# Kernel tuning notes

Measured on AMD Instinct MI355X. Metric: run time of the kernel, lower is better.

The kernel has to match this reference:

```python
import jax, jax.numpy as jnp
import numpy as np

B, S, D, H, P = 4, 4096, 1024, 8, 32
K = D // H  # head_dim = 128


def setup_inputs() -> dict:
    key = jax.random.key(0)
    ks = jax.random.split(key, 12)
    f = lambda k, shape, s: jax.random.normal(k, shape, dtype=jnp.float32) * s
    return {
        "x": f(ks[0], (B, S, D), 1.0),
        "W_proj": f(ks[1], (H, K, D), 0.03),
        "resonance_freqs": f(ks[2], (H, K), 0.01),
        "pol_W": f(ks[3], (H, P, K), 0.08),
        "pol_b": jnp.zeros((H, P), jnp.float32),
        "imp_W1": f(ks[4], (16, 1), 0.5),               # Linear(1, 16)
        "imp_b1": jnp.zeros((16,), jnp.float32),
        "imp_W2": f(ks[5], (1, 16), 0.25),              # Linear(16, 1)
        "imp_b2": jnp.zeros((1,), jnp.float32),
        "out_W": f(ks[6], (D, D), 0.03),                # Linear(dim, dim)
        "out_b": jnp.zeros((D,), jnp.float32),
        "ln_g": jnp.ones((D,), jnp.float32),
        "ln_b": jnp.zeros((D,), jnp.float32),
        "causal": 1,
    }


def reference(x, W_proj, resonance_freqs, pol_W, pol_b, imp_W1, imp_b1,
              imp_W2, imp_b2, out_W, out_b, ln_g, ln_b, causal):
    Bx, Sx, Dx = x.shape
    nH = W_proj.shape[0]
    # per-head projection + resonance frequency modulation -> (B, H, S, K)
    heads = jnp.einsum('bsd,hkd->bhsk', x, W_proj)
    heads = heads * jnp.cos(resonance_freqs * jnp.pi)[None, :, None, :]

    # --- GuaXiangDuiChong: learned cross-head impedance ---
    summary = heads.mean(axis=2)                                   # (B, H, K)
    pol = jnp.tanh(jnp.einsum('bhk,hpk->bhp', summary, pol_W) + pol_b[None])
    pol = pol / jnp.maximum(jnp.linalg.norm(pol, axis=-1, keepdims=True), 1e-12)
    dots = jnp.einsum('bhp,bgp->bhg', pol, pol)                    # (B, H, H)
    z = dots[..., None]                                            # (B, H, H, 1)
    hid = jax.nn.gelu(z * imp_W1[:, 0] + imp_b1, approximate=False)  # (B, H, H, 16)
    imp = jax.nn.softplus(jnp.einsum('bijc,oc->bijo', hid, imp_W2) + imp_b2)[..., 0]
    eye = jnp.eye(nH, dtype=x.dtype)
    impedance = imp * (1.0 - eye)                                  # (B, H, H)

    # --- cross-head transfer ---
    # h_i += sum_{j != i} heads_j / (1 + imp[i,j]) * 0.1, causally mean-masked.
    coef = (0.1 / (1.0 + impedance)) * (1.0 - eye)                 # zero diagonal (i == j skipped)
    transfer = jnp.einsum('bij,bjsk->bisk', coef, heads)           # (B, H, S, K)
    if causal and Sx > 1:
        # masked_fill(t>s)+mean over t of a key-independent tensor == scale by (s+1)/S
        scale = (jnp.arange(Sx, dtype=x.dtype) + 1.0) / Sx
        transfer = transfer * scale[None, None, :, None]
    out_heads = heads + transfer

    merged = out_heads.transpose(0, 2, 1, 3).reshape(Bx, Sx, Dx)   # cat heads on last dim
    y = merged @ out_W.T + out_b + x                               # dropout is identity in eval
    mu = y.mean(-1, keepdims=True)
    var = ((y - mu) ** 2).mean(-1, keepdims=True)
    normed = (y - mu) / jnp.sqrt(var + 1e-5) * ln_g + ln_b
    return normed, impedance
```

## Files before the change

kernel.cpp:

```cpp
#include <hip/hip_runtime.h>

typedef __bf16 bf16x8 __attribute__((ext_vector_type(8)));
typedef float f32x4 __attribute__((ext_vector_type(4)));

#define PI_F 3.14159265358979323846f

__device__ __forceinline__ unsigned short f2bf(float f) {
    unsigned u = __float_as_uint(f);
    u += 0x7FFFu + ((u >> 16) & 1u);
    return (unsigned short)(u >> 16);
}
__device__ __forceinline__ float bf2f(unsigned short h) {
    return __uint_as_float(((unsigned)h) << 16);
}

__device__ __forceinline__ void async16(const void* g, void* l) {
    __builtin_amdgcn_global_load_lds(
        (const __attribute__((address_space(1))) unsigned int*)g,
        (__attribute__((address_space(3))) unsigned int*)l, 16, 0, 0);
}

__global__ __launch_bounds__(256) void prep_w1(const float* __restrict__ W,
                                               const float* __restrict__ fr,
                                               unsigned short* __restrict__ W1b) {
    int idx = blockIdx.x * 256 + threadIdx.x;
    int n = idx >> 10, d = idx & 1023;
    int k = n >> 3, h = n & 7;
    float c = cosf(fr[h * 128 + k] * PI_F);
    W1b[idx] = f2bf(W[((h * 128 + k) << 10) + d] * c);
}

__global__ __launch_bounds__(256) void prep_wo(const float* __restrict__ Wo,
                                               unsigned short* __restrict__ Wob) {
    int idx = blockIdx.x * 256 + threadIdx.x;
    int n = idx >> 10, dp = idx & 1023;
    int k = dp >> 3, h = dp & 7;
    Wob[idx] = f2bf(Wo[(n << 10) + h * 128 + k]);
}

__global__ __launch_bounds__(256) void xbar_cast(const float* __restrict__ x,
                                                 unsigned short* __restrict__ xb,
                                                 float* __restrict__ xbar) {
    int bid = blockIdx.x;
    int b = bid >> 7;
    int s0 = (bid & 127) * 32;
    int t = threadIdx.x;
    float a0 = 0.f, a1 = 0.f, a2 = 0.f, a3 = 0.f;
    for (int i = 0; i < 32; ++i) {
        long row = (long)b * 4096 + s0 + i;
        float4 v = ((const float4*)x)[row * 256 + t];
        a0 += v.x; a1 += v.y; a2 += v.z; a3 += v.w;
        ushort4 u;
        u.x = f2bf(v.x); u.y = f2bf(v.y); u.z = f2bf(v.z); u.w = f2bf(v.w);
        ((ushort4*)xb)[row * 256 + t] = u;
    }
    float* xr = xbar + b * 1024 + t * 4;
    atomicAdd(xr + 0, a0); atomicAdd(xr + 1, a1);
    atomicAdd(xr + 2, a2); atomicAdd(xr + 3, a3);
}

__global__ __launch_bounds__(256) void summary_k(const float* __restrict__ xbar,
                                                 const float* __restrict__ W,
                                                 const float* __restrict__ fr,
                                                 float* __restrict__ summary) {
    int wave = (blockIdx.x * 256 + threadIdx.x) >> 6;
    int lane = threadIdx.x & 63;
    int b = wave >> 10, hk = wave & 1023;
    int h = hk >> 7, k = hk & 127;
    const float* wrow = &W[(h * 128 + k) << 10];
    const float* xrow = &xbar[b << 10];
    float s = 0.f;
    for (int d = lane; d < 1024; d += 64) s += xrow[d] * wrow[d];
    for (int off = 32; off; off >>= 1) s += __shfl_down(s, off);
    if (lane == 0) {
        float c = cosf(fr[h * 128 + k] * PI_F);
        summary[wave] = s * c * (1.0f / 4096.0f);
    }
}

__global__ __launch_bounds__(256) void imp_k(const float* __restrict__ summary,
                                             const float* __restrict__ pol_W,
                                             const float* __restrict__ pol_b,
                                             const float* __restrict__ imp_W1,
                                             const float* __restrict__ imp_b1,
                                             const float* __restrict__ imp_W2,
                                             const float* __restrict__ imp_b2,
                                             float* __restrict__ coef_out,
                                             float* __restrict__ imp_out) {
    __shared__ float pol[4][8][32];
    __shared__ float rn[32];
    int t = threadIdx.x;
    for (int o = t; o < 1024; o += 256) {
        int b = o >> 8, h = (o >> 5) & 7, p = o & 31;
        const float* srow = &summary[(b * 8 + h) * 128];
        const float* wrow = &pol_W[(h * 32 + p) * 128];
        float acc = pol_b[h * 32 + p];
        for (int k = 0; k < 128; ++k) acc += srow[k] * wrow[k];
        pol[b][h][p] = tanhf(acc);
    }
    __syncthreads();
    if (t < 32) {
        int b = t >> 3, h = t & 7;
        float ss = 0.f;
        for (int p = 0; p < 32; ++p) { float v = pol[b][h][p]; ss += v * v; }
        rn[t] = 1.0f / fmaxf(sqrtf(ss), 1e-12f);
    }
    __syncthreads();
    {
        int b = t >> 6, i = (t >> 3) & 7, j = t & 7;
        float d = 0.f;
        for (int p = 0; p < 32; ++p) d += pol[b][i][p] * pol[b][j][p];
        d *= rn[b * 8 + i] * rn[b * 8 + j];
        float s = imp_b2[0];
        for (int c = 0; c < 16; ++c) {
            float z = d * imp_W1[c] + imp_b1[c];
            float gl = 0.5f * z * (1.0f + erff(z * 0.70710678118654752f));
            s += gl * imp_W2[c];
        }
        float sp = fmaxf(s, 0.0f) + log1pf(expf(-fabsf(s)));
        float impv = (i == j) ? 0.0f : sp;
        imp_out[t] = impv;
        coef_out[t] = (i == j) ? 0.0f : 0.1f / (1.0f + impv);
    }
}

__global__ __launch_bounds__(256, 3) void gemm_bt(const unsigned short* __restrict__ A,
                                                  const unsigned short* __restrict__ B,
                                                  unsigned short* __restrict__ C) {
    __shared__ unsigned short As[128 * 32];
    __shared__ unsigned short Bs[128 * 32];
    const int t = threadIdx.x;
    const int wave = t >> 6;
    const int lane = t & 63;
    const int wr = wave >> 1, wc = wave & 1;
    const long rowBase = (long)blockIdx.y * 128;
    const long colBase = (long)blockIdx.x * 128;

    const int lr = lane >> 2;
    const int lb = (lane & 3) * 16;
    const char* gA = (const char*)A + (rowBase + wave * 32 + lr) * 2048 + lb;
    const char* gB = (const char*)B + (colBase + wave * 32 + lr) * 2048 + lb;
    char* lA = (char*)As + wave * 2048;
    char* lB = (char*)Bs + wave * 2048;
    const int q = lane >> 4;
    const int c16 = lane & 15;

    f32x4 acc[4][4] = {};
    for (int kt = 0; kt < 1024; kt += 32) {
        const char* a0 = gA + kt * 2;
        const char* b0 = gB + kt * 2;
        async16(a0, lA);
        async16(a0 + 16 * 2048, lA + 1024);
        async16(b0, lB);
        async16(b0 + 16 * 2048, lB + 1024);
        __syncthreads();
        bf16x8 af[4], bfr[4];
#pragma unroll
        for (int mi = 0; mi < 4; ++mi)
            af[mi] = *(const bf16x8*)((const char*)As + ((wr * 64 + mi * 16 + c16) * 32 + q * 8) * 2);
#pragma unroll
        for (int ni = 0; ni < 4; ++ni)
            bfr[ni] = *(const bf16x8*)((const char*)Bs + ((wc * 64 + ni * 16 + c16) * 32 + q * 8) * 2);
#pragma unroll
        for (int mi = 0; mi < 4; ++mi)
#pragma unroll
            for (int ni = 0; ni < 4; ++ni)
                acc[mi][ni] = __builtin_amdgcn_mfma_f32_16x16x32_bf16(af[mi], bfr[ni], acc[mi][ni], 0, 0, 0);
        __syncthreads();
    }
#pragma unroll
    for (int mi = 0; mi < 4; ++mi) {
#pragma unroll
        for (int ni = 0; ni < 4; ++ni) {
            long col = colBase + wc * 64 + ni * 16 + c16;
            long row0 = rowBase + wr * 64 + mi * 16 + q * 4;
#pragma unroll
            for (int r = 0; r < 4; ++r)
                C[(row0 + r) * 1024 + col] = f2bf(acc[mi][ni][r]);
        }
    }
}

__global__ __launch_bounds__(256) void mix_k(const unsigned short* __restrict__ heads,
                                             const float* __restrict__ coef,
                                             const int* __restrict__ causal,
                                             unsigned short* __restrict__ merged) {
    __shared__ float cf[256];
    int t = threadIdx.x;
    cf[t] = coef[t];
    __syncthreads();
    long g = (long)blockIdx.x * 256 + t;
    long bs = g >> 7;
    int m = (int)(g & 127);
    int b = (int)(bs >> 12);
    int s = (int)(bs & 4095);
    float scale = causal[0] ? (float)(s + 1) * (1.0f / 4096.0f) : 1.0f;
    const ushort4* hp = (const ushort4*)(heads + bs * 1024 + m * 8);
    ushort4 u0 = hp[0], u1 = hp[1];
    float v[8] = {bf2f(u0.x), bf2f(u0.y), bf2f(u0.z), bf2f(u0.w),
                  bf2f(u1.x), bf2f(u1.y), bf2f(u1.z), bf2f(u1.w)};
    const float* cb = cf + b * 64;
    float o[8];
#pragma unroll
    for (int i = 0; i < 8; ++i) {
        float ts = 0.f;
#pragma unroll
        for (int j = 0; j < 8; ++j) ts += cb[i * 8 + j] * v[j];
        o[i] = v[i] + scale * ts;
    }
    ushort4 o0, o1;
    o0.x = f2bf(o[0]); o0.y = f2bf(o[1]); o0.z = f2bf(o[2]); o0.w = f2bf(o[3]);
    o1.x = f2bf(o[4]); o1.y = f2bf(o[5]); o1.z = f2bf(o[6]); o1.w = f2bf(o[7]);
    ushort4* op = (ushort4*)(merged + bs * 1024 + m * 8);
    op[0] = o0; op[1] = o1;
}

__global__ __launch_bounds__(256) void ln_k(const unsigned short* __restrict__ ypre,
                                            const float* __restrict__ x,
                                            const float* __restrict__ outb,
                                            const float* __restrict__ gam,
                                            const float* __restrict__ bet,
                                            float* __restrict__ out) {
    int row = blockIdx.x;
    int t = threadIdx.x;
    long base = (long)row * 1024 + t * 4;
    ushort4 yp = *(const ushort4*)(ypre + base);
    float4 xv = *(const float4*)(x + base);
    float4 bv = *(const float4*)(outb + t * 4);
    float y0 = bf2f(yp.x) + xv.x + bv.x;
    float y1 = bf2f(yp.y) + xv.y + bv.y;
    float y2 = bf2f(yp.z) + xv.z + bv.z;
    float y3 = bf2f(yp.w) + xv.w + bv.w;
    float s = y0 + y1 + y2 + y3;
    float ss = y0 * y0 + y1 * y1 + y2 * y2 + y3 * y3;
    for (int off = 32; off; off >>= 1) {
        s += __shfl_down(s, off);
        ss += __shfl_down(ss, off);
    }
    __shared__ float red[8];
    int wv = t >> 6, ln = t & 63;
    if (ln == 0) { red[wv] = s; red[4 + wv] = ss; }
    __syncthreads();
    if (t == 0) {
        float S1 = red[0] + red[1] + red[2] + red[3];
        float S2 = red[4] + red[5] + red[6] + red[7];
        float mu = S1 * (1.0f / 1024.0f);
        float var = S2 * (1.0f / 1024.0f) - mu * mu;
        red[0] = mu;
        red[1] = 1.0f / sqrtf(var + 1e-5f);
    }
    __syncthreads();
    float mu = red[0], rs = red[1];
    float4 gv = *(const float4*)(gam + t * 4);
    float4 bb = *(const float4*)(bet + t * 4);
    float4 o;
    o.x = (y0 - mu) * rs * gv.x + bb.x;
    o.y = (y1 - mu) * rs * gv.y + bb.y;
    o.z = (y2 - mu) * rs * gv.z + bb.z;
    o.w = (y3 - mu) * rs * gv.w + bb.w;
    *(float4*)(out + base) = o;
}

extern "C" void kernel_launch(void* const* d_in, const int* in_sizes, int n_in,
                              void* d_out, int out_size, void* d_ws, size_t ws_size,
                              hipStream_t stream) {
    const float* x       = (const float*)d_in[0];
    const float* W_proj  = (const float*)d_in[1];
    const float* freqs   = (const float*)d_in[2];
    const float* pol_W   = (const float*)d_in[3];
    const float* pol_b   = (const float*)d_in[4];
    const float* imp_W1  = (const float*)d_in[5];
    const float* imp_b1  = (const float*)d_in[6];
    const float* imp_W2  = (const float*)d_in[7];
    const float* imp_b2  = (const float*)d_in[8];
    const float* out_W   = (const float*)d_in[9];
    const float* out_b   = (const float*)d_in[10];
    const float* ln_g    = (const float*)d_in[11];
    const float* ln_b    = (const float*)d_in[12];
    const int*   causal  = (const int*)d_in[13];
    float* out = (float*)d_out;

    char* ws = (char*)d_ws;
    unsigned short* xb      = (unsigned short*)(ws + 0);
    unsigned short* heads   = (unsigned short*)(ws + 33554432);
    unsigned short* w1b     = (unsigned short*)(ws + 67108864);
    unsigned short* wob     = (unsigned short*)(ws + 69206016);
    float* xbar             = (float*)(ws + 71303168);
    float* summary          = (float*)(ws + 71319552);
    float* coef             = (float*)(ws + 71335936);
    unsigned short* merged  = xb;
    unsigned short* ypre    = heads;

    hipMemsetAsync(xbar, 0, 4096 * sizeof(float), stream);
    prep_w1<<<4096, 256, 0, stream>>>(W_proj, freqs, w1b);
    prep_wo<<<4096, 256, 0, stream>>>(out_W, wob);
    xbar_cast<<<512, 256, 0, stream>>>(x, xb, xbar);
    summary_k<<<1024, 256, 0, stream>>>(xbar, W_proj, freqs, summary);
    imp_k<<<1, 256, 0, stream>>>(summary, pol_W, pol_b, imp_W1, imp_b1,
                                 imp_W2, imp_b2, coef, out + 16777216);
    gemm_bt<<<dim3(8, 128), 256, 0, stream>>>(xb, w1b, heads);
    mix_k<<<8192, 256, 0, stream>>>(heads, coef, causal, merged);
    gemm_bt<<<dim3(8, 128), 256, 0, stream>>>(merged, wob, ypre);
    ln_k<<<16384, 256, 0, stream>>>(ypre, x, out_b, ln_g, ln_b, out);
}
```

Measured before the change: 319.9 us.

## Fuse head mixing into first GEMM epilogue, deepen K tile with swizzled LDS

```diff
diff --git a/kernel.cpp b/kernel.cpp
--- a/kernel.cpp
+++ b/kernel.cpp
@@ -2,6 +2,7 @@
 
 typedef __bf16 bf16x8 __attribute__((ext_vector_type(8)));
 typedef float f32x4 __attribute__((ext_vector_type(4)));
+typedef unsigned short us8 __attribute__((ext_vector_type(8)));
 
 #define PI_F 3.14159265358979323846f
 
@@ -20,33 +21,34 @@
         (__attribute__((address_space(3))) unsigned int*)l, 16, 0, 0);
 }
 
-__global__ __launch_bounds__(256) void prep_w1(const float* __restrict__ W,
-                                               const float* __restrict__ fr,
-                                               unsigned short* __restrict__ W1b) {
+__global__ __launch_bounds__(256) void prep_k(const float* __restrict__ W,
+                                              const float* __restrict__ fr,
+                                              const float* __restrict__ Wo,
+                                              unsigned short* __restrict__ W1b,
+                                              unsigned short* __restrict__ Wob) {
     int idx = blockIdx.x * 256 + threadIdx.x;
-    int n = idx >> 10, d = idx & 1023;
-    int k = n >> 3, h = n & 7;
-    float c = cosf(fr[h * 128 + k] * PI_F);
-    W1b[idx] = f2bf(W[((h * 128 + k) << 10) + d] * c);
-}
-
-__global__ __launch_bounds__(256) void prep_wo(const float* __restrict__ Wo,
-                                               unsigned short* __restrict__ Wob) {
-    int idx = blockIdx.x * 256 + threadIdx.x;
-    int n = idx >> 10, dp = idx & 1023;
-    int k = dp >> 3, h = dp & 7;
-    Wob[idx] = f2bf(Wo[(n << 10) + h * 128 + k]);
+    if (idx < (1 << 20)) {
+        int n = idx >> 10, d = idx & 1023;
+        int k = n >> 3, h = n & 7;
+        float c = cosf(fr[h * 128 + k] * PI_F);
+        W1b[idx] = f2bf(W[((h * 128 + k) << 10) + d] * c);
+    } else {
+        int i2 = idx - (1 << 20);
+        int n = i2 >> 10, dp = i2 & 1023;
+        int k = dp >> 3, h = dp & 7;
+        Wob[i2] = f2bf(Wo[(n << 10) + h * 128 + k]);
+    }
 }
 
 __global__ __launch_bounds__(256) void xbar_cast(const float* __restrict__ x,
                                                  unsigned short* __restrict__ xb,
                                                  float* __restrict__ xbar) {
     int bid = blockIdx.x;
-    int b = bid >> 7;
-    int s0 = (bid & 127) * 32;
+    int b = bid >> 9;
+    int s0 = (bid & 511) * 8;
     int t = threadIdx.x;
     float a0 = 0.f, a1 = 0.f, a2 = 0.f, a3 = 0.f;
-    for (int i = 0; i < 32; ++i) {
+    for (int i = 0; i < 8; ++i) {
         long row = (long)b * 4096 + s0 + i;
         float4 v = ((const float4*)x)[row * 256 + t];
         a0 += v.x; a1 += v.y; a2 += v.z; a3 += v.w;
@@ -124,50 +126,131 @@
     }
 }
 
+__device__ __forceinline__ void swizzle_blk(int n, long& rowBase, long& colBase) {
+    int xcd = n & 7, s = n >> 3;
+    rowBase = (long)(xcd * 16 + (s & 15)) * 128;
+    colBase = (long)(s >> 4) * 128;
+}
+
+#define GEMM_CORE(A_, B_, As_, Bs_)                                            \
+    const int wave = t >> 6;                                                   \
+    const int lane = t & 63;                                                   \
+    const int wr = wave >> 1, wc = wave & 1;                                   \
+    const int lr8 = lane >> 3;                             \
+    const int gr = lane & 7;                                      \
+    const int sw = ((gr ^ lr8) << 4);    \
+    const char* gA = (const char*)A_ + (rowBase + wave * 32 + lr8) * 2048 + sw;\
+    const char* gB = (const char*)B_ + (colBase + wave * 32 + lr8) * 2048 + sw;\
+    char* lA = (char*)As_ + wave * 4096;                                       \
+    char* lB = (char*)Bs_ + wave * 4096;                                       \
+    const int q = lane >> 4;                                                   \
+    const int c16 = lane & 15;                                                 \
+    const int xorm = c16 & 7;                                                  \
+    const int oA0 = ((q ^ xorm) << 4);                 \
+    const int oA1 = (((4 + q) ^ xorm) << 4);           \
+    const int aRow = (wr * 64 + c16) * 128;                                    \
+    const int bRow = (wc * 64 + c16) * 128;                                    \
+    f32x4 acc[4][4] = {};                                                      \
+    for (int kt = 0; kt < 2048; kt += 128) {                                   \
+        const char* a0 = gA + kt;                                              \
+        const char* b0 = gB + kt;                                              \
+        async16(a0, lA);                                                       \
+        async16(a0 + 8 * 2048, lA + 1024);                                     \
+        async16(a0 + 16 * 2048, lA + 2048);                                    \
+        async16(a0 + 24 * 2048, lA + 3072);                                    \
+        async16(b0, lB);                                                       \
+        async16(b0 + 8 * 2048, lB + 1024);                                     \
+        async16(b0 + 16 * 2048, lB + 2048);                                    \
+        async16(b0 + 24 * 2048, lB + 3072);                                    \
+        __syncthreads();                                                       \
+        bf16x8 af[2][4], bfr[2][4];                                            \
+        _Pragma("unroll")                                                      \
+        for (int mi = 0; mi < 4; ++mi) {                                       \
+            af[0][mi] = *(const bf16x8*)((const char*)As_ + aRow + mi * 2048 + oA0); \
+            af[1][mi] = *(const bf16x8*)((const char*)As_ + aRow + mi * 2048 + oA1); \
+        }                                                                      \
+        _Pragma("unroll")                                                      \
+        for (int ni = 0; ni < 4; ++ni) {                                       \
+            bfr[0][ni] = *(const bf16x8*)((const char*)Bs_ + bRow + ni * 2048 + oA0); \
+            bfr[1][ni] = *(const bf16x8*)((const char*)Bs_ + bRow + ni * 2048 + oA1); \
+        }                                                                      \
+        _Pragma("unroll")                                                      \
+        for (int h = 0; h < 2; ++h)                                            \
+            _Pragma("unroll")                                                  \
+            for (int mi = 0; mi < 4; ++mi)                                     \
+                _Pragma("unroll")                                              \
+                for (int ni = 0; ni < 4; ++ni)                                 \
+                    acc[mi][ni] = __builtin_amdgcn_mfma_f32_16x16x32_bf16(     \
+                        af[h][mi], bfr[h][ni], acc[mi][ni], 0, 0, 0);          \
+        __syncthreads();                                                       \
+    }
+
+__global__ __launch_bounds__(256, 3) void gemm1_mix(const unsigned short* __restrict__ A,
+                                                    const unsigned short* __restrict__ B,
+                                                    const float* __restrict__ coef,
+                                                    const int* __restrict__ causal,
+                                                    unsigned short* __restrict__ C) {
+    __shared__ float mixs[64 * 132];
+    __shared__ float cfs[64];
+    unsigned short* As = (unsigned short*)mixs;
+    unsigned short* Bs = As + 8192;
+    const int t = threadIdx.x;
+    long rowBase, colBase;
+    swizzle_blk(blockIdx.x, rowBase, colBase);
+    const int b = (int)(rowBase >> 12);
+    if (t < 64) cfs[t] = coef[b * 64 + t];
+    const int causalv = causal[0];
+
+    GEMM_CORE(A, B, As, Bs)
+
+#pragma unroll
+    for (int pass = 0; pass < 2; ++pass) {
+        if (wr == pass) {
+#pragma unroll
+            for (int mi = 0; mi < 4; ++mi)
+#pragma unroll
+                for (int ni = 0; ni < 4; ++ni)
+#pragma unroll
+                    for (int r = 0; r < 4; ++r)
+                        mixs[(mi * 16 + q * 4 + r) * 132 + wc * 64 + ni * 16 + c16] = acc[mi][ni][r];
+        }
+        __syncthreads();
+        long rb2 = rowBase + pass * 64;
+#pragma unroll
+        for (int it = 0; it < 4; ++it) {
+            int item = t + it * 256;
+            int r = item >> 4, kg = item & 15;
+            const float* src = mixs + r * 132 + kg * 8;
+            float v[8];
+#pragma unroll
+            for (int j = 0; j < 8; ++j) v[j] = src[j];
+            long row = rb2 + r;
+            float scale = causalv ? (float)((row & 4095) + 1) * (1.0f / 4096.0f) : 1.0f;
+            us8 o;
+#pragma unroll
+            for (int i = 0; i < 8; ++i) {
+                float ts = 0.f;
+#pragma unroll
+                for (int j = 0; j < 8; ++j) ts += cfs[i * 8 + j] * v[j];
+                o[i] = f2bf(v[i] + scale * ts);
+            }
+            *(us8*)(C + row * 1024 + colBase + kg * 8) = o;
+        }
+        __syncthreads();
+    }
+}
+
 __global__ __launch_bounds__(256, 3) void gemm_bt(const unsigned short* __restrict__ A,
                                                   const unsigned short* __restrict__ B,
                                                   unsigned short* __restrict__ C) {
-    __shared__ unsigned short As[128 * 32];
-    __shared__ unsigned short Bs[128 * 32];
+    __shared__ unsigned short As[128 * 64];
+    __shared__ unsigned short Bs[128 * 64];
     const int t = threadIdx.x;
-    const int wave = t >> 6;
-    const int lane = t & 63;
-    const int wr = wave >> 1, wc = wave & 1;
-    const long rowBase = (long)blockIdx.y * 128;
-    const long colBase = (long)blockIdx.x * 128;
-
-    const int lr = lane >> 2;
-    const int lb = (lane & 3) * 16;
-    const char* gA = (const char*)A + (rowBase + wave * 32 + lr) * 2048 + lb;
-    const char* gB = (const char*)B + (colBase + wave * 32 + lr) * 2048 + lb;
-    char* lA = (char*)As + wave * 2048;
-    char* lB = (char*)Bs + wave * 2048;
-    const int q = lane >> 4;
-    const int c16 = lane & 15;
-
-    f32x4 acc[4][4] = {};
-    for (int kt = 0; kt < 1024; kt += 32) {
-        const char* a0 = gA + kt * 2;
-        const char* b0 = gB + kt * 2;
-        async16(a0, lA);
-        async16(a0 + 16 * 2048, lA + 1024);
-        async16(b0, lB);
-        async16(b0 + 16 * 2048, lB + 1024);
-        __syncthreads();
-        bf16x8 af[4], bfr[4];
-#pragma unroll
-        for (int mi = 0; mi < 4; ++mi)
-            af[mi] = *(const bf16x8*)((const char*)As + ((wr * 64 + mi * 16 + c16) * 32 + q * 8) * 2);
-#pragma unroll
-        for (int ni = 0; ni < 4; ++ni)
-            bfr[ni] = *(const bf16x8*)((const char*)Bs + ((wc * 64 + ni * 16 + c16) * 32 + q * 8) * 2);
-#pragma unroll
-        for (int mi = 0; mi < 4; ++mi)
-#pragma unroll
-            for (int ni = 0; ni < 4; ++ni)
-                acc[mi][ni] = __builtin_amdgcn_mfma_f32_16x16x32_bf16(af[mi], bfr[ni], acc[mi][ni], 0, 0, 0);
-        __syncthreads();
-    }
+    long rowBase, colBase;
+    swizzle_blk(blockIdx.x, rowBase, colBase);
+
+    GEMM_CORE(A, B, As, Bs)
+
 #pragma unroll
     for (int mi = 0; mi < 4; ++mi) {
 #pragma unroll
@@ -179,40 +262,6 @@
                 C[(row0 + r) * 1024 + col] = f2bf(acc[mi][ni][r]);
         }
     }
-}
-
-__global__ __launch_bounds__(256) void mix_k(const unsigned short* __restrict__ heads,
-                                             const float* __restrict__ coef,
-                                             const int* __restrict__ causal,
-                                             unsigned short* __restrict__ merged) {
-    __shared__ float cf[256];
-    int t = threadIdx.x;
-    cf[t] = coef[t];
-    __syncthreads();
-    long g = (long)blockIdx.x * 256 + t;
-    long bs = g >> 7;
-    int m = (int)(g & 127);
-    int b = (int)(bs >> 12);
-    int s = (int)(bs & 4095);
-    float scale = causal[0] ? (float)(s + 1) * (1.0f / 4096.0f) : 1.0f;
-    const ushort4* hp = (const ushort4*)(heads + bs * 1024 + m * 8);
-    ushort4 u0 = hp[0], u1 = hp[1];
-    float v[8] = {bf2f(u0.x), bf2f(u0.y), bf2f(u0.z), bf2f(u0.w),
-                  bf2f(u1.x), bf2f(u1.y), bf2f(u1.z), bf2f(u1.w)};
-    const float* cb = cf + b * 64;
-    float o[8];
-#pragma unroll
-    for (int i = 0; i < 8; ++i) {
-        float ts = 0.f;
-#pragma unroll
-        for (int j = 0; j < 8; ++j) ts += cb[i * 8 + j] * v[j];
-        o[i] = v[i] + scale * ts;
-    }
-    ushort4 o0, o1;
-    o0.x = f2bf(o[0]); o0.y = f2bf(o[1]); o0.z = f2bf(o[2]); o0.w = f2bf(o[3]);
-    o1.x = f2bf(o[4]); o1.y = f2bf(o[5]); o1.z = f2bf(o[6]); o1.w = f2bf(o[7]);
-    ushort4* op = (ushort4*)(merged + bs * 1024 + m * 8);
-    op[0] = o0; op[1] = o1;
 }
 
 __global__ __launch_bounds__(256) void ln_k(const unsigned short* __restrict__ ypre,
@@ -282,24 +331,21 @@
 
     char* ws = (char*)d_ws;
     unsigned short* xb      = (unsigned short*)(ws + 0);
-    unsigned short* heads   = (unsigned short*)(ws + 33554432);
+    unsigned short* merged  = (unsigned short*)(ws + 33554432);
     unsigned short* w1b     = (unsigned short*)(ws + 67108864);
     unsigned short* wob     = (unsigned short*)(ws + 69206016);
     float* xbar             = (float*)(ws + 71303168);
     float* summary          = (float*)(ws + 71319552);
     float* coef             = (float*)(ws + 71335936);
-    unsigned short* merged  = xb;
-    unsigned short* ypre    = heads;
+    unsigned short* ypre    = xb;
 
     hipMemsetAsync(xbar, 0, 4096 * sizeof(float), stream);
-    prep_w1<<<4096, 256, 0, stream>>>(W_proj, freqs, w1b);
-    prep_wo<<<4096, 256, 0, stream>>>(out_W, wob);
-    xbar_cast<<<512, 256, 0, stream>>>(x, xb, xbar);
+    prep_k<<<8192, 256, 0, stream>>>(W_proj, freqs, out_W, w1b, wob);
+    xbar_cast<<<2048, 256, 0, stream>>>(x, xb, xbar);
     summary_k<<<1024, 256, 0, stream>>>(xbar, W_proj, freqs, summary);
     imp_k<<<1, 256, 0, stream>>>(summary, pol_W, pol_b, imp_W1, imp_b1,
                                  imp_W2, imp_b2, coef, out + 16777216);
-    gemm_bt<<<dim3(8, 128), 256, 0, stream>>>(xb, w1b, heads);
-    mix_k<<<8192, 256, 0, stream>>>(heads, coef, causal, merged);
-    gemm_bt<<<dim3(8, 128), 256, 0, stream>>>(merged, wob, ypre);
+    gemm1_mix<<<1024, 256, 0, stream>>>(xb, w1b, coef, causal, merged);
+    gemm_bt<<<1024, 256, 0, stream>>>(merged, wob, ypre);
     ln_k<<<16384, 256, 0, stream>>>(ypre, x, out_b, ln_g, ln_b, out);
 }
```

After: 403.2 us. 26.0% more time.

## Merge weight-prep kernels, replace atomic mean with two-stage reduction, swizzle GEMM tiles

Applied to the files above, without the earlier changes.

```diff
diff --git a/kernel.cpp b/kernel.cpp
--- a/kernel.cpp
+++ b/kernel.cpp
@@ -2,6 +2,7 @@
 
 typedef __bf16 bf16x8 __attribute__((ext_vector_type(8)));
 typedef float f32x4 __attribute__((ext_vector_type(4)));
+typedef unsigned short us8 __attribute__((ext_vector_type(8)));
 
 #define PI_F 3.14159265358979323846f
 
@@ -20,33 +21,34 @@
         (__attribute__((address_space(3))) unsigned int*)l, 16, 0, 0);
 }
 
-__global__ __launch_bounds__(256) void prep_w1(const float* __restrict__ W,
-                                               const float* __restrict__ fr,
-                                               unsigned short* __restrict__ W1b) {
+__global__ __launch_bounds__(256) void prep_k(const float* __restrict__ W,
+                                              const float* __restrict__ fr,
+                                              const float* __restrict__ Wo,
+                                              unsigned short* __restrict__ W1b,
+                                              unsigned short* __restrict__ Wob) {
     int idx = blockIdx.x * 256 + threadIdx.x;
-    int n = idx >> 10, d = idx & 1023;
-    int k = n >> 3, h = n & 7;
-    float c = cosf(fr[h * 128 + k] * PI_F);
-    W1b[idx] = f2bf(W[((h * 128 + k) << 10) + d] * c);
-}
-
-__global__ __launch_bounds__(256) void prep_wo(const float* __restrict__ Wo,
-                                               unsigned short* __restrict__ Wob) {
-    int idx = blockIdx.x * 256 + threadIdx.x;
-    int n = idx >> 10, dp = idx & 1023;
-    int k = dp >> 3, h = dp & 7;
-    Wob[idx] = f2bf(Wo[(n << 10) + h * 128 + k]);
+    if (idx < (1 << 20)) {
+        int n = idx >> 10, d = idx & 1023;
+        int k = n >> 3, h = n & 7;
+        float c = cosf(fr[h * 128 + k] * PI_F);
+        W1b[idx] = f2bf(W[((h * 128 + k) << 10) + d] * c);
+    } else {
+        int i2 = idx - (1 << 20);
+        int n = i2 >> 10, dp = i2 & 1023;
+        int k = dp >> 3, h = dp & 7;
+        Wob[i2] = f2bf(Wo[(n << 10) + h * 128 + k]);
+    }
 }
 
 __global__ __launch_bounds__(256) void xbar_cast(const float* __restrict__ x,
                                                  unsigned short* __restrict__ xb,
-                                                 float* __restrict__ xbar) {
+                                                 float* __restrict__ part) {
     int bid = blockIdx.x;
-    int b = bid >> 7;
-    int s0 = (bid & 127) * 32;
+    int b = bid >> 8;
+    int s0 = (bid & 255) * 16;
     int t = threadIdx.x;
     float a0 = 0.f, a1 = 0.f, a2 = 0.f, a3 = 0.f;
-    for (int i = 0; i < 32; ++i) {
+    for (int i = 0; i < 16; ++i) {
         long row = (long)b * 4096 + s0 + i;
         float4 v = ((const float4*)x)[row * 256 + t];
         a0 += v.x; a1 += v.y; a2 += v.z; a3 += v.w;
@@ -54,9 +56,26 @@
         u.x = f2bf(v.x); u.y = f2bf(v.y); u.z = f2bf(v.z); u.w = f2bf(v.w);
         ((ushort4*)xb)[row * 256 + t] = u;
     }
-    float* xr = xbar + b * 1024 + t * 4;
-    atomicAdd(xr + 0, a0); atomicAdd(xr + 1, a1);
-    atomicAdd(xr + 2, a2); atomicAdd(xr + 3, a3);
+    float4 p; p.x = a0; p.y = a1; p.z = a2; p.w = a3;
+    ((float4*)part)[bid * 256 + t] = p;
+}
+
+__global__ __launch_bounds__(256) void xbar_r(const float* __restrict__ part,
+                                              float* __restrict__ xbar) {
+    __shared__ float sl[256];
+    int blk = blockIdx.x;
+    int b = blk >> 3, dgrp = blk & 7;
+    int t = threadIdx.x;
+    int col = dgrp * 128 + (t & 127);
+    int ih = t >> 7;
+    float s = 0.f;
+    for (int i = 0; i < 128; ++i) {
+        int cb = b * 256 + ih * 128 + i;
+        s += part[cb * 1024 + col];
+    }
+    sl[t] = s;
+    __syncthreads();
+    if (t < 128) xbar[b * 1024 + col] = sl[t] + sl[t + 128];
 }
 
 __global__ __launch_bounds__(256) void summary_k(const float* __restrict__ xbar,
@@ -124,6 +143,12 @@
     }
 }
 
+__device__ __forceinline__ void swizzle_blk(int n, long& rowBase, long& colBase) {
+    int xcd = n & 7, s = n >> 3;
+    rowBase = (long)(xcd * 16 + (s & 15)) * 128;
+    colBase = (long)(s >> 4) * 128;
+}
+
 __global__ __launch_bounds__(256, 3) void gemm_bt(const unsigned short* __restrict__ A,
                                                   const unsigned short* __restrict__ B,
                                                   unsigned short* __restrict__ C) {
@@ -133,8 +158,8 @@
     const int wave = t >> 6;
     const int lane = t & 63;
     const int wr = wave >> 1, wc = wave & 1;
-    const long rowBase = (long)blockIdx.y * 128;
-    const long colBase = (long)blockIdx.x * 128;
+    long rowBase, colBase;
+    swizzle_blk(blockIdx.x, rowBase, colBase);
 
     const int lr = lane >> 2;
     const int lb = (lane & 3) * 16;
@@ -241,16 +266,11 @@
     int wv = t >> 6, ln = t & 63;
     if (ln == 0) { red[wv] = s; red[4 + wv] = ss; }
     __syncthreads();
-    if (t == 0) {
-        float S1 = red[0] + red[1] + red[2] + red[3];
-        float S2 = red[4] + red[5] + red[6] + red[7];
-        float mu = S1 * (1.0f / 1024.0f);
-        float var = S2 * (1.0f / 1024.0f) - mu * mu;
-        red[0] = mu;
-        red[1] = 1.0f / sqrtf(var + 1e-5f);
-    }
-    __syncthreads();
-    float mu = red[0], rs = red[1];
+    float S1 = red[0] + red[1] + red[2] + red[3];
+    float S2 = red[4] + red[5] + red[6] + red[7];
+    float mu = S1 * (1.0f / 1024.0f);
+    float var = S2 * (1.0f / 1024.0f) - mu * mu;
+    float rs = 1.0f / sqrtf(var + 1e-5f);
     float4 gv = *(const float4*)(gam + t * 4);
     float4 bb = *(const float4*)(bet + t * 4);
     float4 o;
@@ -288,18 +308,18 @@
     float* xbar             = (float*)(ws + 71303168);
     float* summary          = (float*)(ws + 71319552);
     float* coef             = (float*)(ws + 71335936);
+    float* part             = (float*)heads;
     unsigned short* merged  = xb;
     unsigned short* ypre    = heads;
 
-    hipMemsetAsync(xbar, 0, 4096 * sizeof(float), stream);
-    prep_w1<<<4096, 256, 0, stream>>>(W_proj, freqs, w1b);
-    prep_wo<<<4096, 256, 0, stream>>>(out_W, wob);
-    xbar_cast<<<512, 256, 0, stream>>>(x, xb, xbar);
+    prep_k<<<8192, 256, 0, stream>>>(W_proj, freqs, out_W, w1b, wob);
+    xbar_cast<<<1024, 256, 0, stream>>>(x, xb, part);
+    xbar_r<<<32, 256, 0, stream>>>(part, xbar);
     summary_k<<<1024, 256, 0, stream>>>(xbar, W_proj, freqs, summary);
     imp_k<<<1, 256, 0, stream>>>(summary, pol_W, pol_b, imp_W1, imp_b1,
                                  imp_W2, imp_b2, coef, out + 16777216);
-    gemm_bt<<<dim3(8, 128), 256, 0, stream>>>(xb, w1b, heads);
+    gemm_bt<<<1024, 256, 0, stream>>>(xb, w1b, heads);
     mix_k<<<8192, 256, 0, stream>>>(heads, coef, causal, merged);
-    gemm_bt<<<dim3(8, 128), 256, 0, stream>>>(merged, wob, ypre);
+    gemm_bt<<<1024, 256, 0, stream>>>(merged, wob, ypre);
     ln_k<<<16384, 256, 0, stream>>>(ypre, x, out_b, ln_g, ln_b, out);
 }
```

New measurement: 303.1 us. -5.2%, faster.
